# Kernel tuning notes

Measured on AMD Instinct MI355X. Metric: run time of the kernel, lower is better.

The kernel has to match this reference:

```python
import jax, jax.numpy as jnp
import numpy as np


def setup_inputs() -> dict:
    key = jax.random.key(0)
    ks = jax.random.split(key, 6)
    B, T, I, H = 64, 4096, 128, 256
    x = jax.random.normal(ks[0], (B, T, I), dtype=jnp.float32)
    W_in = jax.random.normal(ks[1], (H, I), dtype=jnp.float32) * (1.0 / np.sqrt(I))
    b_in = jax.random.normal(ks[2], (H,), dtype=jnp.float32) * 0.01
    W_rec = jax.random.normal(ks[3], (H, H), dtype=jnp.float32) * (1.0 / np.sqrt(H))
    b_rec = jax.random.normal(ks[4], (H,), dtype=jnp.float32) * 0.01
    tau = jax.random.uniform(ks[5], (H,), dtype=jnp.float32)  # clamped to [0.1, 5] in forward
    return {"x": x, "W_in": W_in, "b_in": b_in, "W_rec": W_rec,
            "b_rec": b_rec, "tau": tau, "num_layers": 2}


def reference(x, W_in, b_in, W_rec, b_rec, tau, num_layers):
    # x: [B, T, I]; returns final hidden state h: [B, H]
    dt = jnp.float32(0.1)
    tau_c = jnp.clip(tau, 0.1, 5.0)                      # [H]
    scale = dt / tau_c                                   # [H]
    # Input projection is identical for every inner iteration -> precompute once.
    x_proj = jnp.einsum('bti,hi->bth', x, W_in) + b_in   # [B, T, H]
    B = x.shape[0]
    H = tau.shape[0]

    def step(h, xt):  # xt: [B, H]
        for _ in range(num_layers):  # small fixed inner loop
            act = jnp.tanh(xt + h @ W_rec.T + b_rec)
            h = h + scale * (act - h)
        return h, None

    h0 = jnp.zeros((B, H), dtype=x.dtype)
    h, _ = jax.lax.scan(step, h0, jnp.swapaxes(x_proj, 0, 1))  # scan over T
    return h
```

## Files before the change

### kernel.cpp

```cpp
#include <hip/hip_runtime.h>


typedef _Float16 half8 __attribute__((ext_vector_type(8)));
typedef _Float16 half4 __attribute__((ext_vector_type(4)));
typedef float    f32x4 __attribute__((ext_vector_type(4)));

#define LGKM_BARRIER() asm volatile("s_waitcnt lgkmcnt(0)\n\ts_barrier" ::: "memory")

__device__ __forceinline__ half8 cvt8s(float4 v0, float4 v1, float s) {
    half8 hv;
    hv[0]=(_Float16)(v0.x*s); hv[1]=(_Float16)(v0.y*s);
    hv[2]=(_Float16)(v0.z*s); hv[3]=(_Float16)(v0.w*s);
    hv[4]=(_Float16)(v1.x*s); hv[5]=(_Float16)(v1.y*s);
    hv[6]=(_Float16)(v1.z*s); hv[7]=(_Float16)(v1.w*s);
    return hv;
}
__device__ __forceinline__ half4 cvt4(float4 v) {
    half4 hv;
    hv[0]=(_Float16)v.x; hv[1]=(_Float16)v.y;
    hv[2]=(_Float16)v.z; hv[3]=(_Float16)v.w;
    return hv;
}

__device__ __forceinline__ float sel4(const f32x4 (&a)[4], int k) {
    float v0 = (k & 2) ? a[2][0] : a[0][0];
    float v1 = (k & 2) ? a[3][0] : a[1][0];
    return (k & 1) ? v1 : v0;
}

__global__ void __launch_bounds__(256, 1)
ltc_fused(const float* __restrict__ x,
          const float* __restrict__ W_in,
          const float* __restrict__ b_in,
          const float* __restrict__ W_rec,
          const float* __restrict__ b_rec,
          const float* __restrict__ tau,
          const int*   __restrict__ num_layers,
          float*       __restrict__ out,
          int T)
{
    const int b    = blockIdx.x;
    const int tid  = threadIdx.x;
    const int lane = tid & 63;
    const int g    = tid >> 6;
    const int n    = lane & 15;
    const int q    = lane >> 4;
    const int L    = num_layers[0];
    const int mycol = 64*g + 16*q + n;
    const unsigned shamt = (unsigned)((q & 1) << 4);

    __shared__ _Float16 hbuf[2][256];
    __shared__ _Float16 xstage[2][16][16][8];
    __shared__ _Float16 pchunk[32][4][16][4];

    const float PRE = 2.8853900817779268f;
    half8 bh[4][8];
    half8 bx[4][4];
    float biasv[4];
#pragma unroll
    for (int t4 = 0; t4 < 4; ++t4) {
        const int col = 64*g + 16*t4 + n;
        const float* rp = &W_rec[col * 256 + 8*q];
#pragma unroll
        for (int i = 0; i < 8; ++i)
            bh[t4][i] = cvt8s(*(const float4*)&rp[32*i],
                              *(const float4*)&rp[32*i + 4], PRE);
        const float* ip = &W_in[col * 128 + 8*q];
#pragma unroll
        for (int i = 0; i < 4; ++i)
            bx[t4][i] = cvt8s(*(const float4*)&ip[32*i],
                              *(const float4*)&ip[32*i + 4], PRE);
        biasv[t4] = (b_in[col] + b_rec[col]) * PRE;
    }
    const float sj   = 0.1f / fminf(fmaxf(tau[mycol], 0.1f), 5.0f);
    const float nsj2 = -2.0f * sj;
    float hj = 0.0f;

    hbuf[0][tid] = (_Float16)0.0f;

    const float* xb  = x + (size_t)b * T * 128;
    const int    t_u = tid >> 3;
    const int    c8  = tid & 7;
    const int    Mts = t_u >> 4, ms = t_u & 15;

    float4 xpre0, xpre1, xpre2, xpre3;
    {
        int tg = t_u; if (tg > T - 1) tg = T - 1;
        const float4* src = (const float4*)(xb + (size_t)tg * 128 + 16*c8);
        xpre0 = src[0]; xpre1 = src[1]; xpre2 = src[2]; xpre3 = src[3];
    }

#define LAYER(RB, WB, XCQ)                                                   \
    do {                                                                     \
        half8 ah[8];                                                         \
        _Pragma("unroll")                                                    \
        for (int i = 0; i < 8; ++i)                                          \
            ah[i] = *(const half8*)&hbuf[RB][32*i + 8*q];                    \
        const float term1 = __builtin_fmaf(sj, 1.0f - hj, hj);               \
        const f32x4 zz = (f32x4){0.f, 0.f, 0.f, 0.f};                        \
        f32x4 A0[4], A1[4], A2[4], A3[4];                                    \
        _Pragma("unroll")                                                    \
        for (int t4 = 0; t4 < 4; ++t4) {                                     \
            A0[t4] = __builtin_amdgcn_mfma_f32_16x16x32_f16(                 \
                ah[0], bh[t4][0], zz, 0, 0, 0);                              \
            A1[t4] = __builtin_amdgcn_mfma_f32_16x16x32_f16(                 \
                ah[2], bh[t4][2], zz, 0, 0, 0);                              \
            A2[t4] = __builtin_amdgcn_mfma_f32_16x16x32_f16(                 \
                ah[4], bh[t4][4], zz, 0, 0, 0);                              \
            A3[t4] = __builtin_amdgcn_mfma_f32_16x16x32_f16(                 \
                ah[6], bh[t4][6], zz, 0, 0, 0);                              \
        }                                                                    \
        _Pragma("unroll")                                                    \
        for (int t4 = 0; t4 < 4; ++t4) {                                     \
            A0[t4] = __builtin_amdgcn_mfma_f32_16x16x32_f16(                 \
                ah[1], bh[t4][1], A0[t4], 0, 0, 0);                          \
            A1[t4] = __builtin_amdgcn_mfma_f32_16x16x32_f16(                 \
                ah[3], bh[t4][3], A1[t4], 0, 0, 0);                          \
            A2[t4] = __builtin_amdgcn_mfma_f32_16x16x32_f16(                 \
                ah[5], bh[t4][5], A2[t4], 0, 0, 0);                          \
            A3[t4] = __builtin_amdgcn_mfma_f32_16x16x32_f16(                 \
                ah[7], bh[t4][7], A3[t4], 0, 0, 0);                          \
        }                                                                    \
        float z = ((sel4(A0, q) + sel4(A1, q))                               \
                 + (sel4(A2, q) + sel4(A3, q))) + (XCQ);                     \
        float e  = __builtin_amdgcn_exp2f(z);         \
        float rr = __builtin_amdgcn_rcpf(e + 1.0f);                          \
        hj = __builtin_fmaf(nsj2, rr, term1);            \
        hbuf[WB][mycol] = (_Float16)hj;                                      \
        LGKM_BARRIER();                                                      \
    } while (0)

    if (L == 2) {
        for (int tc = 0; tc < T; tc += 32) {
            *(half4*)&xstage[Mts][2*c8    ][ms][0] = cvt4(xpre0);
            *(half4*)&xstage[Mts][2*c8    ][ms][4] = cvt4(xpre1);
            *(half4*)&xstage[Mts][2*c8 + 1][ms][0] = cvt4(xpre2);
            *(half4*)&xstage[Mts][2*c8 + 1][ms][4] = cvt4(xpre3);
            __syncthreads();

#pragma unroll
            for (int Mt = 0; Mt < 2; ++Mt) {
                half8 ax[4];
#pragma unroll
                for (int ks = 0; ks < 4; ++ks)
                    ax[ks] = *(const half8*)&xstage[Mt][4*ks + q][n][0];
                f32x4 pa[4];
#pragma unroll
                for (int t4 = 0; t4 < 4; ++t4)
                    pa[t4] = (f32x4){biasv[t4], biasv[t4], biasv[t4], biasv[t4]};
#pragma unroll
                for (int ks = 0; ks < 4; ++ks)
#pragma unroll
                    for (int t4 = 0; t4 < 4; ++t4)
                        pa[t4] = __builtin_amdgcn_mfma_f32_16x16x32_f16(
                            ax[ks], bx[t4][ks], pa[t4], 0, 0, 0);
#pragma unroll
                for (int r = 0; r < 4; ++r) {
                    half4 pk;
                    pk[0] = (_Float16)pa[0][r]; pk[1] = (_Float16)pa[1][r];
                    pk[2] = (_Float16)pa[2][r]; pk[3] = (_Float16)pa[3][r];
                    *(half4*)&pchunk[16*Mt + 4*q + r][g][n][0] = pk;
                }
            }
            __syncthreads();

            {
                const int nc = (tc + 32 < T) ? tc + 32 : tc;
                int tg = nc + t_u; if (tg > T - 1) tg = T - 1;
                const float4* src = (const float4*)(xb + (size_t)tg * 128 + 16*c8);
                xpre0 = src[0]; xpre1 = src[1]; xpre2 = src[2]; xpre3 = src[3];
            }

            const int tlen = (T - tc < 32) ? (T - tc) : 32;
#pragma unroll 2
            for (int ts = 0; ts < tlen; ++ts) {
                const uint2 pv = *(const uint2*)&pchunk[ts][g][n][0];
                unsigned d = (q & 2) ? pv.y : pv.x;
                d >>= shamt;
                float xcq;
                { union { unsigned u; _Float16 h[2]; } uu; uu.u = d;
                  xcq = (float)uu.h[0]; }

                LAYER(0, 1, xcq);
                LAYER(1, 0, xcq);
            }
        }
    } else {
        int hb = 0;
        for (int tc = 0; tc < T; tc += 32) {
            *(half4*)&xstage[Mts][2*c8    ][ms][0] = cvt4(xpre0);
            *(half4*)&xstage[Mts][2*c8    ][ms][4] = cvt4(xpre1);
            *(half4*)&xstage[Mts][2*c8 + 1][ms][0] = cvt4(xpre2);
            *(half4*)&xstage[Mts][2*c8 + 1][ms][4] = cvt4(xpre3);
            __syncthreads();

#pragma unroll
            for (int Mt = 0; Mt < 2; ++Mt) {
                half8 ax[4];
#pragma unroll
                for (int ks = 0; ks < 4; ++ks)
                    ax[ks] = *(const half8*)&xstage[Mt][4*ks + q][n][0];
                f32x4 pa[4];
#pragma unroll
                for (int t4 = 0; t4 < 4; ++t4)
                    pa[t4] = (f32x4){biasv[t4], biasv[t4], biasv[t4], biasv[t4]};
#pragma unroll
                for (int ks = 0; ks < 4; ++ks)
#pragma unroll
                    for (int t4 = 0; t4 < 4; ++t4)
                        pa[t4] = __builtin_amdgcn_mfma_f32_16x16x32_f16(
                            ax[ks], bx[t4][ks], pa[t4], 0, 0, 0);
#pragma unroll
                for (int r = 0; r < 4; ++r) {
                    half4 pk;
                    pk[0] = (_Float16)pa[0][r]; pk[1] = (_Float16)pa[1][r];
                    pk[2] = (_Float16)pa[2][r]; pk[3] = (_Float16)pa[3][r];
                    *(half4*)&pchunk[16*Mt + 4*q + r][g][n][0] = pk;
                }
            }
            __syncthreads();

            {
                const int nc = (tc + 32 < T) ? tc + 32 : tc;
                int tg = nc + t_u; if (tg > T - 1) tg = T - 1;
                const float4* src = (const float4*)(xb + (size_t)tg * 128 + 16*c8);
                xpre0 = src[0]; xpre1 = src[1]; xpre2 = src[2]; xpre3 = src[3];
            }

            const int tlen = (T - tc < 32) ? (T - tc) : 32;
            for (int ts = 0; ts < tlen; ++ts) {
                const uint2 pv = *(const uint2*)&pchunk[ts][g][n][0];
                unsigned d = (q & 2) ? pv.y : pv.x;
                d >>= shamt;
                float xcq;
                { union { unsigned u; _Float16 h[2]; } uu; uu.u = d;
                  xcq = (float)uu.h[0]; }

                for (int l = 0; l < L; ++l) {
                    if (hb == 0) LAYER(0, 1, xcq);
                    else         LAYER(1, 0, xcq);
                    hb ^= 1;
                }
            }
        }
    }
#undef LAYER

    out[(size_t)b * 256 + mycol] = hj;
}

extern "C" void kernel_launch(void* const* d_in, const int* in_sizes, int n_in,
                              void* d_out, int out_size, void* d_ws, size_t ws_size,
                              hipStream_t stream) {
    const float* x     = (const float*)d_in[0];
    const float* W_in  = (const float*)d_in[1];
    const float* b_in  = (const float*)d_in[2];
    const float* W_rec = (const float*)d_in[3];
    const float* b_rec = (const float*)d_in[4];
    const float* tau   = (const float*)d_in[5];
    const int*   numl  = (const int*)d_in[6];

    const int H = in_sizes[2];
    const int I = in_sizes[1] / H;
    const int B = out_size / H;
    const int T = in_sizes[0] / (B * I);

    ltc_fused<<<B, 256, 0, stream>>>(x, W_in, b_in, W_rec, b_rec, tau,
                                     numl, (float*)d_out, T);
}
```

Measured before the change: 3.314 ms.

## Split recurrent columns across 8 wavefronts instead of 4 per block

Doubles the block to 512 threads so each wavefront owns 32 hidden columns instead of 64, halving the MFMA chain per wave per layer step, and cuts the input-projection MFMAs per wave the same way. The per-step critical path through the matrix unit is meant to shrink. In exchange every step's barrier now synchronises twice as many waves, and half the lanes compute duplicate values that are written redundantly to shared memory. Staging and prefetch of x are reshaped to match the new thread count.

Measured after the change: 3.237 ms. 1.02x faster.

```diff
diff --git a/kernel.cpp b/kernel.cpp
--- a/kernel.cpp
+++ b/kernel.cpp
@@ -2,7 +2,6 @@
 
 
 typedef _Float16 half8 __attribute__((ext_vector_type(8)));
-typedef _Float16 half4 __attribute__((ext_vector_type(4)));
 typedef float    f32x4 __attribute__((ext_vector_type(4)));
 
 #define LGKM_BARRIER() asm volatile("s_waitcnt lgkmcnt(0)\n\ts_barrier" ::: "memory")
@@ -15,20 +14,16 @@
     hv[6]=(_Float16)(v1.z*s); hv[7]=(_Float16)(v1.w*s);
     return hv;
 }
-__device__ __forceinline__ half4 cvt4(float4 v) {
-    half4 hv;
-    hv[0]=(_Float16)v.x; hv[1]=(_Float16)v.y;
-    hv[2]=(_Float16)v.z; hv[3]=(_Float16)v.w;
+__device__ __forceinline__ half8 cvt8(float4 v0, float4 v1) {
+    half8 hv;
+    hv[0]=(_Float16)v0.x; hv[1]=(_Float16)v0.y;
+    hv[2]=(_Float16)v0.z; hv[3]=(_Float16)v0.w;
+    hv[4]=(_Float16)v1.x; hv[5]=(_Float16)v1.y;
+    hv[6]=(_Float16)v1.z; hv[7]=(_Float16)v1.w;
     return hv;
 }
 
-__device__ __forceinline__ float sel4(const f32x4 (&a)[4], int k) {
-    float v0 = (k & 2) ? a[2][0] : a[0][0];
-    float v1 = (k & 2) ? a[3][0] : a[1][0];
-    return (k & 1) ? v1 : v0;
-}
-
-__global__ void __launch_bounds__(256, 1)
+__global__ void __launch_bounds__(512, 2)
 ltc_fused(const float* __restrict__ x,
           const float* __restrict__ W_in,
           const float* __restrict__ b_in,
@@ -45,49 +40,50 @@
     const int g    = tid >> 6;
     const int n    = lane & 15;
     const int q    = lane >> 4;
+    const int t_my = q & 1;
     const int L    = num_layers[0];
-    const int mycol = 64*g + 16*q + n;
-    const unsigned shamt = (unsigned)((q & 1) << 4);
+    const int mycol = 32*g + 16*t_my + n;
+    const unsigned shamt = (unsigned)(t_my << 4);
 
     __shared__ _Float16 hbuf[2][256];
     __shared__ _Float16 xstage[2][16][16][8];
-    __shared__ _Float16 pchunk[32][4][16][4];
+    __shared__ _Float16 pchunk[32][8][16][2];
 
     const float PRE = 2.8853900817779268f;
-    half8 bh[4][8];
-    half8 bx[4][4];
-    float biasv[4];
+    half8 bh[2][8];
+    half8 bx[2][4];
+    float biasv[2];
 #pragma unroll
-    for (int t4 = 0; t4 < 4; ++t4) {
-        const int col = 64*g + 16*t4 + n;
+    for (int t = 0; t < 2; ++t) {
+        const int col = 32*g + 16*t + n;
         const float* rp = &W_rec[col * 256 + 8*q];
 #pragma unroll
         for (int i = 0; i < 8; ++i)
-            bh[t4][i] = cvt8s(*(const float4*)&rp[32*i],
-                              *(const float4*)&rp[32*i + 4], PRE);
+            bh[t][i] = cvt8s(*(const float4*)&rp[32*i],
+                             *(const float4*)&rp[32*i + 4], PRE);
         const float* ip = &W_in[col * 128 + 8*q];
 #pragma unroll
         for (int i = 0; i < 4; ++i)
-            bx[t4][i] = cvt8s(*(const float4*)&ip[32*i],
-                              *(const float4*)&ip[32*i + 4], PRE);
-        biasv[t4] = (b_in[col] + b_rec[col]) * PRE;
+            bx[t][i] = cvt8s(*(const float4*)&ip[32*i],
+                             *(const float4*)&ip[32*i + 4], PRE);
+        biasv[t] = (b_in[col] + b_rec[col]) * PRE;
     }
     const float sj   = 0.1f / fminf(fmaxf(tau[mycol], 0.1f), 5.0f);
     const float nsj2 = -2.0f * sj;
     float hj = 0.0f;
 
-    hbuf[0][tid] = (_Float16)0.0f;
+    if (tid < 256) hbuf[0][tid] = (_Float16)0.0f;
 
     const float* xb  = x + (size_t)b * T * 128;
-    const int    t_u = tid >> 3;
-    const int    c8  = tid & 7;
+    const int    t_u = tid >> 4;
+    const int    c16 = tid & 15;
     const int    Mts = t_u >> 4, ms = t_u & 15;
 
-    float4 xpre0, xpre1, xpre2, xpre3;
+    float4 xpreA, xpreB;
     {
         int tg = t_u; if (tg > T - 1) tg = T - 1;
-        const float4* src = (const float4*)(xb + (size_t)tg * 128 + 16*c8);
-        xpre0 = src[0]; xpre1 = src[1]; xpre2 = src[2]; xpre3 = src[3];
+        const float4* src = (const float4*)(xb + (size_t)tg * 128 + 8*c16);
+        xpreA = src[0]; xpreB = src[1];
     }
 
 #define LAYER(RB, WB, XCQ)                                                   \
@@ -98,89 +94,97 @@
             ah[i] = *(const half8*)&hbuf[RB][32*i + 8*q];                    \
         const float term1 = __builtin_fmaf(sj, 1.0f - hj, hj);               \
         const f32x4 zz = (f32x4){0.f, 0.f, 0.f, 0.f};                        \
-        f32x4 A0[4], A1[4], A2[4], A3[4];                                    \
-        _Pragma("unroll")                                                    \
-        for (int t4 = 0; t4 < 4; ++t4) {                                     \
-            A0[t4] = __builtin_amdgcn_mfma_f32_16x16x32_f16(                 \
-                ah[0], bh[t4][0], zz, 0, 0, 0);                              \
-            A1[t4] = __builtin_amdgcn_mfma_f32_16x16x32_f16(                 \
-                ah[2], bh[t4][2], zz, 0, 0, 0);                              \
-            A2[t4] = __builtin_amdgcn_mfma_f32_16x16x32_f16(                 \
-                ah[4], bh[t4][4], zz, 0, 0, 0);                              \
-            A3[t4] = __builtin_amdgcn_mfma_f32_16x16x32_f16(                 \
-                ah[6], bh[t4][6], zz, 0, 0, 0);                              \
+        f32x4 A0[2], A1[2], A2[2], A3[2];                                    \
+        _Pragma("unroll")                                                    \
+        for (int t = 0; t < 2; ++t) {                                        \
+            A0[t] = __builtin_amdgcn_mfma_f32_16x16x32_f16(                  \
+                ah[0], bh[t][0], zz, 0, 0, 0);                               \
+            A1[t] = __builtin_amdgcn_mfma_f32_16x16x32_f16(                  \
+                ah[2], bh[t][2], zz, 0, 0, 0);                               \
+            A2[t] = __builtin_amdgcn_mfma_f32_16x16x32_f16(                  \
+                ah[4], bh[t][4], zz, 0, 0, 0);                               \
+            A3[t] = __builtin_amdgcn_mfma_f32_16x16x32_f16(                  \
+                ah[6], bh[t][6], zz, 0, 0, 0);                               \
         }                                                                    \
         _Pragma("unroll")                                                    \
-        for (int t4 = 0; t4 < 4; ++t4) {                                     \
-            A0[t4] = __builtin_amdgcn_mfma_f32_16x16x32_f16(                 \
-                ah[1], bh[t4][1], A0[t4], 0, 0, 0);                          \
-            A1[t4] = __builtin_amdgcn_mfma_f32_16x16x32_f16(                 \
-                ah[3], bh[t4][3], A1[t4], 0, 0, 0);                          \
-            A2[t4] = __builtin_amdgcn_mfma_f32_16x16x32_f16(                 \
-                ah[5], bh[t4][5], A2[t4], 0, 0, 0);                          \
-            A3[t4] = __builtin_amdgcn_mfma_f32_16x16x32_f16(                 \
-                ah[7], bh[t4][7], A3[t4], 0, 0, 0);                          \
+        for (int t = 0; t < 2; ++t) {                                        \
+            A0[t] = __builtin_amdgcn_mfma_f32_16x16x32_f16(                  \
+                ah[1], bh[t][1], A0[t], 0, 0, 0);                            \
+            A1[t] = __builtin_amdgcn_mfma_f32_16x16x32_f16(                  \
+                ah[3], bh[t][3], A1[t], 0, 0, 0);                            \
+            A2[t] = __builtin_amdgcn_mfma_f32_16x16x32_f16(                  \
+                ah[5], bh[t][5], A2[t], 0, 0, 0);                            \
+            A3[t] = __builtin_amdgcn_mfma_f32_16x16x32_f16(                  \
+                ah[7], bh[t][7], A3[t], 0, 0, 0);                            \
         }                                                                    \
-        float z = ((sel4(A0, q) + sel4(A1, q))                               \
-                 + (sel4(A2, q) + sel4(A3, q))) + (XCQ);                     \
+        float s0 = t_my ? A0[1][0] : A0[0][0];                               \
+        float s1 = t_my ? A1[1][0] : A1[0][0];                               \
+        float s2 = t_my ? A2[1][0] : A2[0][0];                               \
+        float s3 = t_my ? A3[1][0] : A3[0][0];                               \
+        float z  = ((s0 + s1) + (s2 + s3)) + (XCQ);                          \
         float e  = __builtin_amdgcn_exp2f(z);         \
         float rr = __builtin_amdgcn_rcpf(e + 1.0f);                          \
         hj = __builtin_fmaf(nsj2, rr, term1);            \
-        hbuf[WB][mycol] = (_Float16)hj;                                      \
+        hbuf[WB][mycol] = (_Float16)hj;  \
         LGKM_BARRIER();                                                      \
     } while (0)
 
+#define STAGE_AND_PROJECT()                                                  \
+    do {                                                                     \
+        *(half8*)&xstage[Mts][c16][ms][0] = cvt8(xpreA, xpreB);              \
+        __syncthreads();                                                     \
+        _Pragma("unroll")                                                    \
+        for (int Mt = 0; Mt < 2; ++Mt) {                                     \
+            half8 ax[4];                                                     \
+            _Pragma("unroll")                                                \
+            for (int ks = 0; ks < 4; ++ks)                                   \
+                ax[ks] = *(const half8*)&xstage[Mt][4*ks + q][n][0];         \
+            f32x4 pa[2];                                                     \
+            _Pragma("unroll")                                                \
+            for (int t = 0; t < 2; ++t)                                      \
+                pa[t] = (f32x4){biasv[t], biasv[t], biasv[t], biasv[t]};     \
+            _Pragma("unroll")                                                \
+            for (int ks = 0; ks < 4; ++ks)                                   \
+                _Pragma("unroll")                                            \
+                for (int t = 0; t < 2; ++t)                                  \
+                    pa[t] = __builtin_amdgcn_mfma_f32_16x16x32_f16(          \
+                        ax[ks], bx[t][ks], pa[t], 0, 0, 0);                  \
+            _Pragma("unroll")                                                \
+            for (int r = 0; r < 4; ++r) {                                    \
+                union { _Float16 h[2]; unsigned u; } pk;                     \
+                pk.h[0] = (_Float16)pa[0][r];                                \
+                pk.h[1] = (_Float16)pa[1][r];                                \
+                *(unsigned*)&pchunk[16*Mt + 4*q + r][g][n][0] = pk.u;        \
+            }                                                                \
+        }                                                                    \
+        __syncthreads();                                                     \
+    } while (0)
+
+#define PREFETCH_NEXT()                                                      \
+    do {                                                                     \
+        const int nc = (tc + 32 < T) ? tc + 32 : tc;                         \
+        int tg = nc + t_u; if (tg > T - 1) tg = T - 1;                       \
+        const float4* src = (const float4*)(xb + (size_t)tg * 128 + 8*c16);  \
+        xpreA = src[0]; xpreB = src[1];                                      \
+    } while (0)
+
+#define XCQ_LOAD(TS)                                                         \
+    float xcq;                                                               \
+    {                                                                        \
+        unsigned d = *(const unsigned*)&pchunk[TS][g][n][0];                 \
+        d >>= shamt;                                                         \
+        union { unsigned u; _Float16 h[2]; } uu; uu.u = d;                   \
+        xcq = (float)uu.h[0];                                                \
+    }
+
     if (L == 2) {
         for (int tc = 0; tc < T; tc += 32) {
-            *(half4*)&xstage[Mts][2*c8    ][ms][0] = cvt4(xpre0);
-            *(half4*)&xstage[Mts][2*c8    ][ms][4] = cvt4(xpre1);
-            *(half4*)&xstage[Mts][2*c8 + 1][ms][0] = cvt4(xpre2);
-            *(half4*)&xstage[Mts][2*c8 + 1][ms][4] = cvt4(xpre3);
-            __syncthreads();
-
-#pragma unroll
-            for (int Mt = 0; Mt < 2; ++Mt) {
-                half8 ax[4];
-#pragma unroll
-                for (int ks = 0; ks < 4; ++ks)
-                    ax[ks] = *(const half8*)&xstage[Mt][4*ks + q][n][0];
-                f32x4 pa[4];
-#pragma unroll
-                for (int t4 = 0; t4 < 4; ++t4)
-                    pa[t4] = (f32x4){biasv[t4], biasv[t4], biasv[t4], biasv[t4]};
-#pragma unroll
-                for (int ks = 0; ks < 4; ++ks)
-#pragma unroll
-                    for (int t4 = 0; t4 < 4; ++t4)
-                        pa[t4] = __builtin_amdgcn_mfma_f32_16x16x32_f16(
-                            ax[ks], bx[t4][ks], pa[t4], 0, 0, 0);
-#pragma unroll
-                for (int r = 0; r < 4; ++r) {
-                    half4 pk;
-                    pk[0] = (_Float16)pa[0][r]; pk[1] = (_Float16)pa[1][r];
-                    pk[2] = (_Float16)pa[2][r]; pk[3] = (_Float16)pa[3][r];
-                    *(half4*)&pchunk[16*Mt + 4*q + r][g][n][0] = pk;
-                }
-            }
-            __syncthreads();
-
-            {
-                const int nc = (tc + 32 < T) ? tc + 32 : tc;
-                int tg = nc + t_u; if (tg > T - 1) tg = T - 1;
-                const float4* src = (const float4*)(xb + (size_t)tg * 128 + 16*c8);
-                xpre0 = src[0]; xpre1 = src[1]; xpre2 = src[2]; xpre3 = src[3];
-            }
-
+            STAGE_AND_PROJECT();
+            PREFETCH_NEXT();
             const int tlen = (T - tc < 32) ? (T - tc) : 32;
 #pragma unroll 2
             for (int ts = 0; ts < tlen; ++ts) {
-                const uint2 pv = *(const uint2*)&pchunk[ts][g][n][0];
-                unsigned d = (q & 2) ? pv.y : pv.x;
-                d >>= shamt;
-                float xcq;
-                { union { unsigned u; _Float16 h[2]; } uu; uu.u = d;
-                  xcq = (float)uu.h[0]; }
-
+                XCQ_LOAD(ts);
                 LAYER(0, 1, xcq);
                 LAYER(1, 0, xcq);
             }
@@ -188,54 +192,11 @@
     } else {
         int hb = 0;
         for (int tc = 0; tc < T; tc += 32) {
-            *(half4*)&xstage[Mts][2*c8    ][ms][0] = cvt4(xpre0);
-            *(half4*)&xstage[Mts][2*c8    ][ms][4] = cvt4(xpre1);
-            *(half4*)&xstage[Mts][2*c8 + 1][ms][0] = cvt4(xpre2);
-            *(half4*)&xstage[Mts][2*c8 + 1][ms][4] = cvt4(xpre3);
-            __syncthreads();
-
-#pragma unroll
-            for (int Mt = 0; Mt < 2; ++Mt) {
-                half8 ax[4];
-#pragma unroll
-                for (int ks = 0; ks < 4; ++ks)
-                    ax[ks] = *(const half8*)&xstage[Mt][4*ks + q][n][0];
-                f32x4 pa[4];
-#pragma unroll
-                for (int t4 = 0; t4 < 4; ++t4)
-                    pa[t4] = (f32x4){biasv[t4], biasv[t4], biasv[t4], biasv[t4]};
-#pragma unroll
-                for (int ks = 0; ks < 4; ++ks)
-#pragma unroll
-                    for (int t4 = 0; t4 < 4; ++t4)
-                        pa[t4] = __builtin_amdgcn_mfma_f32_16x16x32_f16(
-                            ax[ks], bx[t4][ks], pa[t4], 0, 0, 0);
-#pragma unroll
-                for (int r = 0; r < 4; ++r) {
-                    half4 pk;
-                    pk[0] = (_Float16)pa[0][r]; pk[1] = (_Float16)pa[1][r];
-                    pk[2] = (_Float16)pa[2][r]; pk[3] = (_Float16)pa[3][r];
-                    *(half4*)&pchunk[16*Mt + 4*q + r][g][n][0] = pk;
-                }
-            }
-            __syncthreads();
-
-            {
-                const int nc = (tc + 32 < T) ? tc + 32 : tc;
-                int tg = nc + t_u; if (tg > T - 1) tg = T - 1;
-                const float4* src = (const float4*)(xb + (size_t)tg * 128 + 16*c8);
-                xpre0 = src[0]; xpre1 = src[1]; xpre2 = src[2]; xpre3 = src[3];
-            }
-
+            STAGE_AND_PROJECT();
+            PREFETCH_NEXT();
             const int tlen = (T - tc < 32) ? (T - tc) : 32;
             for (int ts = 0; ts < tlen; ++ts) {
-                const uint2 pv = *(const uint2*)&pchunk[ts][g][n][0];
-                unsigned d = (q & 2) ? pv.y : pv.x;
-                d >>= shamt;
-                float xcq;
-                { union { unsigned u; _Float16 h[2]; } uu; uu.u = d;
-                  xcq = (float)uu.h[0]; }
-
+                XCQ_LOAD(ts);
                 for (int l = 0; l < L; ++l) {
                     if (hb == 0) LAYER(0, 1, xcq);
                     else         LAYER(1, 0, xcq);
@@ -245,8 +206,12 @@
         }
     }
 #undef LAYER
-
-    out[(size_t)b * 256 + mycol] = hj;
+#undef STAGE_AND_PROJECT
+#undef PREFETCH_NEXT
+#undef XCQ_LOAD
+
+    if (q < 2)
+        out[(size_t)b * 256 + mycol] = hj;
 }
 
 extern "C" void kernel_launch(void* const* d_in, const int* in_sizes, int n_in,
@@ -265,6 +230,6 @@
     const int B = out_size / H;
     const int T = in_sizes[0] / (B * I);
 
-    ltc_fused<<<B, 256, 0, stream>>>(x, W_in, b_in, W_rec, b_rec, tau,
+    ltc_fused<<<B, 512, 0, stream>>>(x, W_in, b_in, W_rec, b_rec, tau,
                                      numl, (float*)d_out, T);
 }
```
